# Performance work log

Measured on AMD Instinct MI355X. Metric: run time of the kernel, lower is better.

Reference implementation:

```python
import jax, jax.numpy as jnp
import numpy as np

M = 128  # split point: first M units use max-plus, rest use min-plus

def setup_inputs() -> dict:
    key = jax.random.key(0)
    k1, k2 = jax.random.split(key)
    x = jax.random.normal(k1, (2048, 512), dtype=jnp.float32)   # (batch, features_in)
    w = jax.random.normal(k2, (512, 256), dtype=jnp.float32)    # (features_in, units)
    return {"x": x, "w": w}

def reference(x, w):
    # Tropical (max/min-plus) pseudo-matmul.
    # s[b, f, u] = x[b, f] + w[f, u]; reduce over f.
    s_max = x[:, :, None] + w[None, :, :M]          # (batch, f, M)
    s_min = x[:, :, None] + w[None, :, M:]          # (batch, f, units-M)
    hv = jnp.max(s_max, axis=1)                     # (batch, M)
    hw = jnp.min(s_min, axis=1)                     # (batch, units-M)
    return jnp.concatenate([hv, hw], axis=1)        # linear activation = identity
```

## Files before the change

### kernel.cpp

```cpp
#include <hip/hip_runtime.h>
#include <math.h>


#define BATCH  2048
#define FEAT   512
#define UNITS  256
#define MSPLIT 128

#define BM 32
#define BN 32
#define BK 64
#define XS_STRIDE 68
#define WS_STRIDE 36

__global__ __launch_bounds__(256, 2) void tropical_mm_kernel(
    const float* __restrict__ x, const float* __restrict__ w, float* __restrict__ out)
{
    __shared__ float xs[BM][XS_STRIDE];
    __shared__ float ws[BK][WS_STRIDE];

    const int tid   = threadIdx.x;
    const int tx    = tid & 15;
    const int ty    = tid >> 4;
    const int ubase = blockIdx.x * BN;
    const int bbase = blockIdx.y * BM;
    const float sgn = (ubase < MSPLIT) ? 1.0f : -1.0f;

    const int xrow = tid >> 4;
    const int xc4  = (tid & 15) << 2;
    const int wrow = tid >> 3;
    const int wc4  = (tid & 7) << 2;

    const int r0 = ty * 2;
    const int r1 = r0 + 1;
    const int c0 = tx * 2;

    float acc00 = -INFINITY, acc01 = -INFINITY;
    float acc10 = -INFINITY, acc11 = -INFINITY;

    for (int k0 = 0; k0 < FEAT; k0 += BK) {
        {
            const float4 v0 = *(const float4*)&x[(size_t)(bbase + xrow)      * FEAT + k0 + xc4];
            const float4 v1 = *(const float4*)&x[(size_t)(bbase + xrow + 16) * FEAT + k0 + xc4];
            *(float4*)&xs[xrow]
                [xc4]      = make_float4(sgn*v0.x, sgn*v0.y, sgn*v0.z, sgn*v0.w);
            *(float4*)&xs[xrow + 16][xc4] = make_float4(sgn*v1.x, sgn*v1.y, sgn*v1.z, sgn*v1.w);
        }
        {
            const float4 v0 = *(const float4*)&w[(size_t)(k0 + wrow)      * UNITS + ubase + wc4];
            const float4 v1 = *(const float4*)&w[(size_t)(k0 + wrow + 32) * UNITS + ubase + wc4];
            *(float4*)&ws[wrow]     [wc4] = make_float4(sgn*v0.x, sgn*v0.y, sgn*v0.z, sgn*v0.w);
            *(float4*)&ws[wrow + 32][wc4] = make_float4(sgn*v1.x, sgn*v1.y, sgn*v1.z, sgn*v1.w);
        }
        __syncthreads();

        #pragma unroll
        for (int kk = 0; kk < BK; kk += 4) {
            const float4 a0 = *(const float4*)&xs[r0][kk];
            const float4 a1 = *(const float4*)&xs[r1][kk];
            const float2 b0 = *(const float2*)&ws[kk + 0][c0];
            const float2 b1 = *(const float2*)&ws[kk + 1][c0];
            const float2 b2 = *(const float2*)&ws[kk + 2][c0];
            const float2 b3 = *(const float2*)&ws[kk + 3][c0];

            acc00 = fmaxf(fmaxf(acc00, a0.x + b0.x), a0.y + b1.x);
            acc00 = fmaxf(fmaxf(acc00, a0.z + b2.x), a0.w + b3.x);
            acc01 = fmaxf(fmaxf(acc01, a0.x + b0.y), a0.y + b1.y);
            acc01 = fmaxf(fmaxf(acc01, a0.z + b2.y), a0.w + b3.y);
            acc10 = fmaxf(fmaxf(acc10, a1.x + b0.x), a1.y + b1.x);
            acc10 = fmaxf(fmaxf(acc10, a1.z + b2.x), a1.w + b3.x);
            acc11 = fmaxf(fmaxf(acc11, a1.x + b0.y), a1.y + b1.y);
            acc11 = fmaxf(fmaxf(acc11, a1.z + b2.y), a1.w + b3.y);
        }
        __syncthreads();
    }

    const size_t obase = (size_t)(bbase + r0) * UNITS + ubase + c0;
    *(float2*)&out[obase]         = make_float2(sgn * acc00, sgn * acc01);
    *(float2*)&out[obase + UNITS] = make_float2(sgn * acc10, sgn * acc11);
}

extern "C" void kernel_launch(void* const* d_in, const int* in_sizes, int n_in,
                              void* d_out, int out_size, void* d_ws, size_t ws_size,
                              hipStream_t stream) {
    const float* x = (const float*)d_in[0];
    const float* w = (const float*)d_in[1];
    float* out = (float*)d_out;

    dim3 grid(UNITS / BN, BATCH / BM);
    dim3 block(256);
    tropical_mm_kernel<<<grid, block, 0, stream>>>(x, w, out);
}
```

Before: 78.72 us.

## Replace LDS-tiled tropical matmul with register-only wavefront-uniform x broadcast kernel

Drops shared memory and barriers entirely. Each lane owns one unit column and each wave owns 8 batch rows, so x loads are wave-uniform (broadcast or scalar-friendly) and w loads coalesce across lanes. Max and min paths are separate template instantiations instead of sign flips, and the reduction is a tree to shorten dependency chains. Reuse now relies on caches rather than LDS, and each thread does one w load per 8 rows, which may raise memory traffic.

```diff
diff --git a/kernel.cpp b/kernel.cpp
--- a/kernel.cpp
+++ b/kernel.cpp
@@ -2,82 +2,73 @@
 #include <math.h>
 
 
-#define BATCH  2048
-#define FEAT   512
-#define UNITS  256
-#define MSPLIT 128
+#define FEAT  512
+#define UNITS 256
+#define TM    8
 
-#define BM 32
-#define BN 32
-#define BK 64
-#define XS_STRIDE 68
-#define WS_STRIDE 36
+template<bool IS_MAX>
+__device__ __forceinline__ void trop_body(const float* __restrict__ x,
+                                          const float* __restrict__ w,
+                                          float* __restrict__ out,
+                                          int ubase) {
+    const int lane = threadIdx.x & 63;
+    const int wv   = __builtin_amdgcn_readfirstlane(threadIdx.x >> 6);
+    const int u    = ubase + lane;
+    const int row0 = blockIdx.y * (4 * TM) + wv * TM;
 
-__global__ __launch_bounds__(256, 2) void tropical_mm_kernel(
-    const float* __restrict__ x, const float* __restrict__ w, float* __restrict__ out)
-{
-    __shared__ float xs[BM][XS_STRIDE];
-    __shared__ float ws[BK][WS_STRIDE];
+    float acc[TM];
+    #pragma unroll
+    for (int r = 0; r < TM; ++r) acc[r] = IS_MAX ? -__builtin_inff() : __builtin_inff();
 
-    const int tid   = threadIdx.x;
-    const int tx    = tid & 15;
-    const int ty    = tid >> 4;
-    const int ubase = blockIdx.x * BN;
-    const int bbase = blockIdx.y * BM;
-    const float sgn = (ubase < MSPLIT) ? 1.0f : -1.0f;
+    const float* wp = w + u;
 
-    const int xrow = tid >> 4;
-    const int xc4  = (tid & 15) << 2;
-    const int wrow = tid >> 3;
-    const int wc4  = (tid & 7) << 2;
-
-    const int r0 = ty * 2;
-    const int r1 = r0 + 1;
-    const int c0 = tx * 2;
-
-    float acc00 = -INFINITY, acc01 = -INFINITY;
-    float acc10 = -INFINITY, acc11 = -INFINITY;
-
-    for (int k0 = 0; k0 < FEAT; k0 += BK) {
-        {
-            const float4 v0 = *(const float4*)&x[(size_t)(bbase + xrow)      * FEAT + k0 + xc4];
-            const float4 v1 = *(const float4*)&x[(size_t)(bbase + xrow + 16) * FEAT + k0 + xc4];
-            *(float4*)&xs[xrow]
-                [xc4]      = make_float4(sgn*v0.x, sgn*v0.y, sgn*v0.z, sgn*v0.w);
-            *(float4*)&xs[xrow + 16][xc4] = make_float4(sgn*v1.x, sgn*v1.y, sgn*v1.z, sgn*v1.w);
-        }
-        {
-            const float4 v0 = *(const float4*)&w[(size_t)(k0 + wrow)      * UNITS + ubase + wc4];
-            const float4 v1 = *(const float4*)&w[(size_t)(k0 + wrow + 32) * UNITS + ubase + wc4];
-            *(float4*)&ws[wrow]     [wc4] = make_float4(sgn*v0.x, sgn*v0.y, sgn*v0.z, sgn*v0.w);
-            *(float4*)&ws[wrow + 32][wc4] = make_float4(sgn*v1.x, sgn*v1.y, sgn*v1.z, sgn*v1.w);
-        }
-        __syncthreads();
+    #pragma unroll 2
+    for (int k0 = 0; k0 < FEAT; k0 += 8) {
+        const float wk0 = wp[(k0 + 0) * UNITS];
+        const float wk1 = wp[(k0 + 1) * UNITS];
+        const float wk2 = wp[(k0 + 2) * UNITS];
+        const float wk3 = wp[(k0 + 3) * UNITS];
+        const float wk4 = wp[(k0 + 4) * UNITS];
+        const float wk5 = wp[(k0 + 5) * UNITS];
+        const float wk6 = wp[(k0 + 6) * UNITS];
+        const float wk7 = wp[(k0 + 7) * UNITS];
 
         #pragma unroll
-        for (int kk = 0; kk < BK; kk += 4) {
-            const float4 a0 = *(const float4*)&xs[r0][kk];
-            const float4 a1 = *(const float4*)&xs[r1][kk];
-            const float2 b0 = *(const float2*)&ws[kk + 0][c0];
-            const float2 b1 = *(const float2*)&ws[kk + 1][c0];
-            const float2 b2 = *(const float2*)&ws[kk + 2][c0];
-            const float2 b3 = *(const float2*)&ws[kk + 3][c0];
+        for (int r = 0; r < TM; ++r) {
+            const float4* xr = (const float4*)(x + (size_t)(row0 + r) * FEAT + k0);
+            const float4 a0 = xr[0];
+            const float4 a1 = xr[1];
 
-            acc00 = fmaxf(fmaxf(acc00, a0.x + b0.x), a0.y + b1.x);
-            acc00 = fmaxf(fmaxf(acc00, a0.z + b2.x), a0.w + b3.x);
-            acc01 = fmaxf(fmaxf(acc01, a0.x + b0.y), a0.y + b1.y);
-            acc01 = fmaxf(fmaxf(acc01, a0.z + b2.y), a0.w + b3.y);
-            acc10 = fmaxf(fmaxf(acc10, a1.x + b0.x), a1.y + b1.x);
-            acc10 = fmaxf(fmaxf(acc10, a1.z + b2.x), a1.w + b3.x);
-            acc11 = fmaxf(fmaxf(acc11, a1.x + b0.y), a1.y + b1.y);
-            acc11 = fmaxf(fmaxf(acc11, a1.z + b2.y), a1.w + b3.y);
+            const float s0 = a0.x + wk0, s1 = a0.y + wk1;
+            const float s2 = a0.z + wk2, s3 = a0.w + wk3;
+            const float s4 = a1.x + wk4, s5 = a1.y + wk5;
+            const float s6 = a1.z + wk6, s7 = a1.w + wk7;
+
+            if (IS_MAX) {
+                const float m0 = fmaxf(fmaxf(s0, s1), s2);
+                const float m1 = fmaxf(fmaxf(s3, s4), s5);
+                const float m2 = fmaxf(fmaxf(s6, s7), acc[r]);
+                acc[r] = fmaxf(fmaxf(m0, m1), m2);
+            } else {
+                const float m0 = fminf(fminf(s0, s1), s2);
+                const float m1 = fminf(fminf(s3, s4), s5);
+                const float m2 = fminf(fminf(s6, s7), acc[r]);
+                acc[r] = fminf(fminf(m0, m1), m2);
+            }
         }
-        __syncthreads();
     }
 
-    const size_t obase = (size_t)(bbase + r0) * UNITS + ubase + c0;
-    *(float2*)&out[obase]         = make_float2(sgn * acc00, sgn * acc01);
-    *(float2*)&out[obase + UNITS] = make_float2(sgn * acc10, sgn * acc11);
+    #pragma unroll
+    for (int r = 0; r < TM; ++r)
+        out[(size_t)(row0 + r) * UNITS + u] = acc[r];
+}
+
+__global__ __launch_bounds__(256) void tropical_kernel(const float* __restrict__ x,
+                                                       const float* __restrict__ w,
+                                                       float* __restrict__ out) {
+    const int ubase = blockIdx.x * 64;
+    if (ubase < 128) trop_body<true>(x, w, out, ubase);
+    else             trop_body<false>(x, w, out, ubase);
 }
 
 extern "C" void kernel_launch(void* const* d_in, const int* in_sizes, int n_in,
@@ -87,7 +78,6 @@
     const float* w = (const float*)d_in[1];
     float* out = (float*)d_out;
 
-    dim3 grid(UNITS / BN, BATCH / BM);
-    dim3 block(256);
-    tropical_mm_kernel<<<grid, block, 0, stream>>>(x, w, out);
+    dim3 grid(UNITS / 64, 2048 / 32);
+    tropical_kernel<<<grid, dim3(256), 0, stream>>>(x, w, out);
 }
```

Measured after the change: 87.28 us. +10.9%, slower.
